# Performance work log

Measured on AMD Instinct MI355X. Metric: run time of the kernel, lower is better.

The kernel has to match this reference:

```python
import jax, jax.numpy as jnp
import numpy as np

NEG_BIG = -9e15

def setup_inputs() -> dict:
    key = jax.random.key(0)
    k1, k2, k3, k4 = jax.random.split(key, 4)
    N, F_in, F_out = 8192, 512, 128
    return {
        "input": jax.random.normal(k1, (N, F_in), dtype=jnp.float32),
        "adj": jax.random.randint(k2, (N, N), 0, 2, dtype=jnp.int32),
        "W": jax.random.normal(k3, (F_in, F_out), dtype=jnp.float32) * 0.05,
        "a": jax.random.normal(k4, (2 * F_out, 1), dtype=jnp.float32) * 0.05,
    }

def reference(input, adj, W, a):
    alpha = 0.2  # LeakyReLU negative slope
    h = input @ W                      # [N, F_out]
    F_out = h.shape[1]
    # concat score decomposition: a^T [h_i || h_j] = h_i @ a1 + h_j @ a2
    a1 = a[:F_out, 0]                  # [F_out]
    a2 = a[F_out:, 0]                  # [F_out]
    e = jax.nn.leaky_relu(h @ a1[:, None] + (h @ a2)[None, :], negative_slope=alpha)  # [N, N]
    e = jnp.where(adj > 0, e, NEG_BIG)
    attention = jax.nn.softmax(e, axis=1)
    h_prime = attention @ h            # [N, F_out]
    return jax.nn.elu(h_prime)         # concat=True
```

## Files before the change

### kernel.cpp

```cpp
#include <hip/hip_runtime.h>
#include <hip/hip_bf16.h>


typedef __attribute__((ext_vector_type(4))) float f32x4;
typedef __attribute__((ext_vector_type(8))) short s16x8;

#define N_NODES 8192
#define F_IN 512
#define F_OUT 128
#define JS 16
#define WCOLS (N_NODES / JS)

static __device__ __forceinline__ short f2bf(float f) {
  __hip_bfloat16 h = __float2bfloat16(f);
  return __builtin_bit_cast(short, h);
}

__global__ __launch_bounds__(256) void k_mask(const int* __restrict__ adj,
    unsigned long long* __restrict__ mask) {
  const int nwaves = gridDim.x * 4;
  int wid = blockIdx.x * 4 + (threadIdx.x >> 6);
  int lane = threadIdx.x & 63;
  const int ntasks = N_NODES * (N_NODES / 256);
  for (int task = wid; task < ntasks; task += nwaves) {
    int row = task >> 5;
    int cg = task & 31;
    const int* p = adj + (size_t)row * N_NODES + cg * 256 + lane;
    int v0 = p[0], v1 = p[64], v2 = p[128], v3 = p[192];
    unsigned long long b0 = __ballot(v0 != 0);
    unsigned long long b1 = __ballot(v1 != 0);
    unsigned long long b2 = __ballot(v2 != 0);
    unsigned long long b3 = __ballot(v3 != 0);
    if (lane == 0) {
      unsigned long long* q = mask + (size_t)row * (N_NODES / 64) + cg * 4;
      ulonglong2 w0; w0.x = b0; w0.y = b1;
      ulonglong2 w1; w1.x = b2; w1.y = b3;
      *(ulonglong2*)(q) = w0;
      *(ulonglong2*)(q + 2) = w1;
    }
  }
}

__global__ void k0a_wt(const float* __restrict__ W, unsigned short* __restrict__ WT) {
  int idx = blockIdx.x * 256 + threadIdx.x;
  int k = idx >> 7, f = idx & 127;
  WT[(size_t)f * F_IN + k] = (unsigned short)f2bf(W[idx]);
}

__global__ void k0c_wa(const float* __restrict__ W, const float* __restrict__ a,
                       float* __restrict__ wa) {
  int k = blockIdx.x * 256 + threadIdx.x;
  if (k >= F_IN) return;
  const float* Wr = W + (size_t)k * F_OUT;
  float d1 = 0.f, d2 = 0.f;
#pragma unroll 8
  for (int f = 0; f < F_OUT; f += 4) {
    f32x4 w  = *(const f32x4*)(Wr + f);
    f32x4 a1 = *(const f32x4*)(a + f);
    f32x4 a2 = *(const f32x4*)(a + F_OUT + f);
    d1 += w[0] * a1[0] + w[1] * a1[1] + w[2] * a1[2] + w[3] * a1[3];
    d2 += w[0] * a2[0] + w[1] * a2[1] + w[2] * a2[2] + w[3] * a2[3];
  }
  wa[k] = d1;
  wa[F_IN + k] = d2;
}

__global__ __launch_bounds__(256) void k0b_x(const float* __restrict__ X,
    const float* __restrict__ wa, unsigned short* __restrict__ Xb,
    f32x4* __restrict__ rowdat, unsigned* __restrict__ pE) {
  int wave = threadIdx.x >> 6, lane = threadIdx.x & 63;
  int i = blockIdx.x * 4 + wave;
  const float* Xr = X + (size_t)i * F_IN + lane * 8;
  f32x4 x0 = ((const f32x4*)Xr)[0];
  f32x4 x1 = ((const f32x4*)Xr)[1];
  f32x4 w10 = ((const f32x4*)(wa + lane * 8))[0];
  f32x4 w11 = ((const f32x4*)(wa + lane * 8))[1];
  f32x4 w20 = ((const f32x4*)(wa + F_IN + lane * 8))[0];
  f32x4 w21 = ((const f32x4*)(wa + F_IN + lane * 8))[1];

  s16x8 xb;
#pragma unroll
  for (int e = 0; e < 4; e++) { xb[e] = f2bf(x0[e]); xb[e + 4] = f2bf(x1[e]); }
  *(s16x8*)(Xb + (size_t)i * F_IN + lane * 8) = xb;

  float d1 = 0.f, d2 = 0.f;
#pragma unroll
  for (int e = 0; e < 4; e++) {
    d1 += x0[e] * w10[e] + x1[e] * w11[e];
    d2 += x0[e] * w20[e] + x1[e] * w21[e];
  }
#pragma unroll
  for (int m = 1; m < 64; m <<= 1) {
    d1 += __shfl_xor(d1, m, 64);
    d2 += __shfl_xor(d2, m, 64);
  }
  if (lane == 0) {
    float s1 = d1, s2 = d2;
    f32x4 rd;
    rd[0] = expf(s1);
    rd[1] = expf(0.2f * s1);
    rd[2] = expf(-s1);
    rd[3] = 0.f;
    rowdat[i] = rd;
    unsigned e2  = (unsigned)(unsigned short)f2bf(expf(s2));
    unsigned e2s = (unsigned)(unsigned short)f2bf(expf(0.2f * s2));
    pE[i] = (e2s << 16) | e2;
  }
}

__global__ __launch_bounds__(256) void k1_gemm(const unsigned short* __restrict__ WT,
    const unsigned short* __restrict__ Xb, unsigned short* __restrict__ hT) {
  int wave = threadIdx.x >> 6, lane = threadIdx.x & 63;
  int lrow = lane & 15, grp = lane >> 4;
  int tile = blockIdx.x * 4 + wave;
  int fb = tile & 7;
  int nb = tile >> 3;

  const unsigned short* Ar = WT + (size_t)(fb * 16 + lrow) * F_IN + grp * 8;
  const unsigned short* Br = Xb + (size_t)(nb * 16 + lrow) * F_IN + grp * 8;

  f32x4 acc = (f32x4)(0.0f);
#pragma unroll
  for (int k0 = 0; k0 < F_IN; k0 += 32) {
    s16x8 af = *(const s16x8*)(Ar + k0);
    s16x8 bf = *(const s16x8*)(Br + k0);
    acc = __builtin_amdgcn_mfma_f32_16x16x32_bf16(af, bf, acc, 0, 0, 0);
  }
#pragma unroll
  for (int r = 0; r < 4; r++)
    hT[(size_t)(fb * 16 + grp * 4 + r) * N_NODES + nb * 16 + lrow] =
        (unsigned short)f2bf(acc[r]);
}

__global__ __launch_bounds__(256, 2) void k2_main(const unsigned* __restrict__ mask32,
    const unsigned short* __restrict__ hT, const f32x4* __restrict__ rowdat,
    const unsigned* __restrict__ pE, float* __restrict__ accws,
    float* __restrict__ denws) {
  int wave = threadIdx.x >> 6, lane = threadIdx.x & 63;
  int lrow = lane & 15, grp = lane >> 4;
  int rb = blockIdx.x >> 2;
  int js = (blockIdx.x & 3) * 4 + wave;
  int rbase = rb * 64;
  int jlo = js * WCOLS;

  float E1[4], E1s[4], T1[4];
#pragma unroll
  for (int rt = 0; rt < 4; rt++) {
    f32x4 rd = rowdat[rbase + rt * 16 + lrow];
    E1[rt] = rd[0]; E1s[rt] = rd[1]; T1[rt] = rd[2];
  }

  f32x4 acc[4][8];
#pragma unroll
  for (int rt = 0; rt < 4; rt++)
#pragma unroll
    for (int n = 0; n < 8; n++) acc[rt][n] = (f32x4)(0.0f);
  float dsum[4] = {0.f, 0.f, 0.f, 0.f};

#define PROC1(rt, pe, e)                                              \
  {                                                                   \
    unsigned pu = (pe);                                               \
    float E2  = __builtin_bit_cast(float, pu << 16);                  \
    float E2s = __builtin_bit_cast(float, pu & 0xffff0000u);          \
    float sel = (E2 > T1[rt]) ? E1[rt] * E2 : E1s[rt] * E2s;          \
    float p = ((b >> (e)) & 1u) ? sel : 0.f;                          \
    dsum[rt] += p;                                                    \
    af[rt][e] = f2bf(p);                                              \
  }

  for (int sc = 0; sc < 4; sc++) {
    int jb = jlo + sc * 128;
    uint4 mm[4];
#pragma unroll
    for (int rt = 0; rt < 4; rt++)
      mm[rt] = *(const uint4*)(mask32 +
          (size_t)(rbase + rt * 16 + lrow) * (N_NODES / 32) + jb / 32);

#pragma unroll
    for (int t = 0; t < 4; t++) {
      int jj = jb + t * 32 + grp * 8;
      const uint4* pp = (const uint4*)(pE + jj);
      uint4 P0 = pp[0], P1 = pp[1];
      s16x8 af[4];
#pragma unroll
      for (int rt = 0; rt < 4; rt++) {
        unsigned b = (mm[rt][t] >> (grp * 8)) & 0xffu;
        PROC1(rt, P0.x, 0); PROC1(rt, P0.y, 1);
        PROC1(rt, P0.z, 2); PROC1(rt, P0.w, 3);
        PROC1(rt, P1.x, 4); PROC1(rt, P1.y, 5);
        PROC1(rt, P1.z, 6); PROC1(rt, P1.w, 7);
      }
#pragma unroll
      for (int n = 0; n < 8; n++) {
        s16x8 bf = *(const s16x8*)(hT + (size_t)(n * 16 + lrow) * N_NODES + jj);
#pragma unroll
        for (int rt = 0; rt < 4; rt++)
          acc[rt][n] =
              __builtin_amdgcn_mfma_f32_16x16x32_bf16(af[rt], bf, acc[rt][n], 0, 0, 0);
      }
    }
  }
#undef PROC1

#pragma unroll
  for (int rt = 0; rt < 4; rt++) {
    float d = dsum[rt];
    d += __shfl_xor(d, 16, 64);
    d += __shfl_xor(d, 32, 64);
    if (lane < 16) denws[js * N_NODES + rbase + rt * 16 + lane] = d;
  }

#pragma unroll
  for (int rt = 0; rt < 4; rt++)
#pragma unroll
    for (int n = 0; n < 8; n++)
#pragma unroll
      for (int r = 0; r < 4; r++)
        accws[((size_t)js * N_NODES + rbase + rt * 16 + grp * 4 + r) * F_OUT +
              n * 16 + lrow] = acc[rt][n][r];
}

__global__ void k3_fin(const float* __restrict__ accws,
                       const float* __restrict__ denws, float* __restrict__ out) {
  int idx4 = blockIdx.x * 256 + threadIdx.x;
  int i = idx4 >> 5;
  const int S4 = N_NODES * F_OUT / 4;
  f32x4 s = (f32x4)(0.0f);
  float d = 0.f;
#pragma unroll
  for (int js = 0; js < JS; js++) {
    s += ((const f32x4*)accws)[idx4 + (size_t)js * S4];
    d += denws[i + js * N_NODES];
  }
  f32x4 v = s / d;
#pragma unroll
  for (int e = 0; e < 4; e++) v[e] = v[e] > 0.f ? v[e] : expm1f(v[e]);
  ((f32x4*)out)[idx4] = v;
}

extern "C" void kernel_launch(void* const* d_in, const int* in_sizes, int n_in,
                              void* d_out, int out_size, void* d_ws, size_t ws_size,
                              hipStream_t stream) {
  const float* X   = (const float*)d_in[0];
  const int*   adj = (const int*)d_in[1];
  const float* W   = (const float*)d_in[2];
  const float* a   = (const float*)d_in[3];
  float* out = (float*)d_out;

  char* ws = (char*)d_ws;
  size_t off = 0;
  unsigned short* WT = (unsigned short*)(ws + off); off += (size_t)F_OUT * F_IN * 2;
  unsigned short* Xb = (unsigned short*)(ws + off); off += (size_t)N_NODES * F_IN * 2;
  unsigned short* hT = (unsigned short*)(ws + off); off += (size_t)F_OUT * N_NODES * 2;
  f32x4* rowdat = (f32x4*)(ws + off); off += (size_t)N_NODES * 16;
  unsigned* pE = (unsigned*)(ws + off); off += (size_t)N_NODES * 4;
  float* wa = (float*)(ws + off); off += (size_t)2 * F_IN * 4;
  unsigned long long* mask = (unsigned long long*)(ws + off);
  off += (size_t)N_NODES * (N_NODES / 64) * 8;
  float* accws = (float*)(ws + off); off += (size_t)JS * N_NODES * F_OUT * 4;
  float* denws = (float*)(ws + off); off += (size_t)JS * N_NODES * 4;
  (void)in_sizes; (void)n_in; (void)out_size; (void)ws_size;

  k_mask<<<2048, 256, 0, stream>>>(adj, mask);
  k0a_wt<<<(F_IN * F_OUT) / 256, 256, 0, stream>>>(W, WT);
  k0c_wa<<<2, 256, 0, stream>>>(W, a, wa);
  k0b_x<<<N_NODES / 4, 256, 0, stream>>>(X, wa, Xb, rowdat, pE);
  k1_gemm<<<1024, 256, 0, stream>>>(WT, Xb, hT);
  k2_main<<<(N_NODES / 64) * (JS / 4), 256, 0, stream>>>((const unsigned*)mask, hT,
                                                         rowdat, pE, accws, denws);
  k3_fin<<<(N_NODES * F_OUT) / 4 / 256, 256, 0, stream>>>(accws, denws, out);
}
```

Measured before the change: 535.8 us.

## Merge prep kernels, drop Xb staging, reduce split-K partials in shared memory

The seven launches become four. The W transpose and the W·a product share one kernel, and the adjacency mask, the row scores and the h GEMM run as disjoint block ranges of a second kernel. The GEMM now reads fp32 X and converts it to bf16 in registers, which removes the Xb buffer and its round trip through memory. The main kernel sums its four waves' partial accumulators in LDS before writing, cutting the accws/denws traffic and the final reduction from 16 slices to 4, at the cost of added LDS and __syncthreads in the epilogue. Merging the mask pass with the GEMM lets them overlap, but the GEMM blocks now redo the fp32 loads and conversions for each feature tile.

```diff
diff --git a/kernel.cpp b/kernel.cpp
--- a/kernel.cpp
+++ b/kernel.cpp
@@ -16,130 +16,132 @@
   return __builtin_bit_cast(short, h);
 }
 
-__global__ __launch_bounds__(256) void k_mask(const int* __restrict__ adj,
-    unsigned long long* __restrict__ mask) {
-  const int nwaves = gridDim.x * 4;
-  int wid = blockIdx.x * 4 + (threadIdx.x >> 6);
-  int lane = threadIdx.x & 63;
-  const int ntasks = N_NODES * (N_NODES / 256);
-  for (int task = wid; task < ntasks; task += nwaves) {
-    int row = task >> 5;
-    int cg = task & 31;
-    const int* p = adj + (size_t)row * N_NODES + cg * 256 + lane;
-    int v0 = p[0], v1 = p[64], v2 = p[128], v3 = p[192];
-    unsigned long long b0 = __ballot(v0 != 0);
-    unsigned long long b1 = __ballot(v1 != 0);
-    unsigned long long b2 = __ballot(v2 != 0);
-    unsigned long long b3 = __ballot(v3 != 0);
+__global__ __launch_bounds__(256) void kA(const float* __restrict__ W,
+    const float* __restrict__ a, unsigned short* __restrict__ WT,
+    float* __restrict__ wa) {
+  int b = blockIdx.x;
+  if (b < 256) {
+    int idx = b * 256 + threadIdx.x;
+    int k = idx >> 7, f = idx & 127;
+    WT[(size_t)f * F_IN + k] = (unsigned short)f2bf(W[idx]);
+  } else {
+    int k = (b - 256) * 256 + threadIdx.x;
+    if (k < F_IN) {
+      const float* Wr = W + (size_t)k * F_OUT;
+      float d1 = 0.f, d2 = 0.f;
+#pragma unroll 8
+      for (int f = 0; f < F_OUT; f += 4) {
+        f32x4 w  = *(const f32x4*)(Wr + f);
+        f32x4 a1 = *(const f32x4*)(a + f);
+        f32x4 a2 = *(const f32x4*)(a + F_OUT + f);
+        d1 += w[0] * a1[0] + w[1] * a1[1] + w[2] * a1[2] + w[3] * a1[3];
+        d2 += w[0] * a2[0] + w[1] * a2[1] + w[2] * a2[2] + w[3] * a2[3];
+      }
+      wa[k] = d1;
+      wa[F_IN + k] = d2;
+    }
+  }
+}
+
+__global__ __launch_bounds__(256) void kB(const int* __restrict__ adj,
+    unsigned long long* __restrict__ mask, const float* __restrict__ X,
+    const float* __restrict__ wa, const unsigned short* __restrict__ WT,
+    f32x4* __restrict__ rowdat, unsigned* __restrict__ pE,
+    unsigned short* __restrict__ hT) {
+  int b = blockIdx.x;
+  int wave = threadIdx.x >> 6, lane = threadIdx.x & 63;
+
+  if (b < 4096) {
+    const int nwaves = 4096 * 4;
+    int wid = b * 4 + wave;
+    const int ntasks = N_NODES * (N_NODES / 256);
+    for (int task = wid; task < ntasks; task += nwaves) {
+      int row = task >> 5;
+      int cg = task & 31;
+      const int* p = adj + (size_t)row * N_NODES + cg * 256 + lane;
+      int v0 = p[0], v1 = p[64], v2 = p[128], v3 = p[192];
+      unsigned long long b0 = __ballot(v0 != 0);
+      unsigned long long b1 = __ballot(v1 != 0);
+      unsigned long long b2 = __ballot(v2 != 0);
+      unsigned long long b3 = __ballot(v3 != 0);
+      if (lane == 0) {
+        unsigned long long* q = mask + (size_t)row * (N_NODES / 64) + cg * 4;
+        ulonglong2 w0; w0.x = b0; w0.y = b1;
+        ulonglong2 w1; w1.x = b2; w1.y = b3;
+        *(ulonglong2*)(q) = w0;
+        *(ulonglong2*)(q + 2) = w1;
+      }
+    }
+  } else if (b < 6144) {
+    int i = (b - 4096) * 4 + wave;
+    const float* Xr = X + (size_t)i * F_IN + lane * 8;
+    f32x4 x0 = ((const f32x4*)Xr)[0];
+    f32x4 x1 = ((const f32x4*)Xr)[1];
+    f32x4 w10 = ((const f32x4*)(wa + lane * 8))[0];
+    f32x4 w11 = ((const f32x4*)(wa + lane * 8))[1];
+    f32x4 w20 = ((const f32x4*)(wa + F_IN + lane * 8))[0];
+    f32x4 w21 = ((const f32x4*)(wa + F_IN + lane * 8))[1];
+    float d1 = 0.f, d2 = 0.f;
+#pragma unroll
+    for (int e = 0; e < 4; e++) {
+      d1 += x0[e] * w10[e] + x1[e] * w11[e];
+      d2 += x0[e] * w20[e] + x1[e] * w21[e];
+    }
+#pragma unroll
+    for (int m = 1; m < 64; m <<= 1) {
+      d1 += __shfl_xor(d1, m, 64);
+      d2 += __shfl_xor(d2, m, 64);
+    }
     if (lane == 0) {
-      unsigned long long* q = mask + (size_t)row * (N_NODES / 64) + cg * 4;
-      ulonglong2 w0; w0.x = b0; w0.y = b1;
-      ulonglong2 w1; w1.x = b2; w1.y = b3;
-      *(ulonglong2*)(q) = w0;
-      *(ulonglong2*)(q + 2) = w1;
-    }
-  }
-}
-
-__global__ void k0a_wt(const float* __restrict__ W, unsigned short* __restrict__ WT) {
-  int idx = blockIdx.x * 256 + threadIdx.x;
-  int k = idx >> 7, f = idx & 127;
-  WT[(size_t)f * F_IN + k] = (unsigned short)f2bf(W[idx]);
-}
-
-__global__ void k0c_wa(const float* __restrict__ W, const float* __restrict__ a,
-                       float* __restrict__ wa) {
-  int k = blockIdx.x * 256 + threadIdx.x;
-  if (k >= F_IN) return;
-  const float* Wr = W + (size_t)k * F_OUT;
-  float d1 = 0.f, d2 = 0.f;
-#pragma unroll 8
-  for (int f = 0; f < F_OUT; f += 4) {
-    f32x4 w  = *(const f32x4*)(Wr + f);
-    f32x4 a1 = *(const f32x4*)(a + f);
-    f32x4 a2 = *(const f32x4*)(a + F_OUT + f);
-    d1 += w[0] * a1[0] + w[1] * a1[1] + w[2] * a1[2] + w[3] * a1[3];
-    d2 += w[0] * a2[0] + w[1] * a2[1] + w[2] * a2[2] + w[3] * a2[3];
-  }
-  wa[k] = d1;
-  wa[F_IN + k] = d2;
-}
-
-__global__ __launch_bounds__(256) void k0b_x(const float* __restrict__ X,
-    const float* __restrict__ wa, unsigned short* __restrict__ Xb,
-    f32x4* __restrict__ rowdat, unsigned* __restrict__ pE) {
-  int wave = threadIdx.x >> 6, lane = threadIdx.x & 63;
-  int i = blockIdx.x * 4 + wave;
-  const float* Xr = X + (size_t)i * F_IN + lane * 8;
-  f32x4 x0 = ((const f32x4*)Xr)[0];
-  f32x4 x1 = ((const f32x4*)Xr)[1];
-  f32x4 w10 = ((const f32x4*)(wa + lane * 8))[0];
-  f32x4 w11 = ((const f32x4*)(wa + lane * 8))[1];
-  f32x4 w20 = ((const f32x4*)(wa + F_IN + lane * 8))[0];
-  f32x4 w21 = ((const f32x4*)(wa + F_IN + lane * 8))[1];
-
-  s16x8 xb;
-#pragma unroll
-  for (int e = 0; e < 4; e++) { xb[e] = f2bf(x0[e]); xb[e + 4] = f2bf(x1[e]); }
-  *(s16x8*)(Xb + (size_t)i * F_IN + lane * 8) = xb;
-
-  float d1 = 0.f, d2 = 0.f;
-#pragma unroll
-  for (int e = 0; e < 4; e++) {
-    d1 += x0[e] * w10[e] + x1[e] * w11[e];
-    d2 += x0[e] * w20[e] + x1[e] * w21[e];
-  }
-#pragma unroll
-  for (int m = 1; m < 64; m <<= 1) {
-    d1 += __shfl_xor(d1, m, 64);
-    d2 += __shfl_xor(d2, m, 64);
-  }
-  if (lane == 0) {
-    float s1 = d1, s2 = d2;
-    f32x4 rd;
-    rd[0] = expf(s1);
-    rd[1] = expf(0.2f * s1);
-    rd[2] = expf(-s1);
-    rd[3] = 0.f;
-    rowdat[i] = rd;
-    unsigned e2  = (unsigned)(unsigned short)f2bf(expf(s2));
-    unsigned e2s = (unsigned)(unsigned short)f2bf(expf(0.2f * s2));
-    pE[i] = (e2s << 16) | e2;
-  }
-}
-
-__global__ __launch_bounds__(256) void k1_gemm(const unsigned short* __restrict__ WT,
-    const unsigned short* __restrict__ Xb, unsigned short* __restrict__ hT) {
-  int wave = threadIdx.x >> 6, lane = threadIdx.x & 63;
-  int lrow = lane & 15, grp = lane >> 4;
-  int tile = blockIdx.x * 4 + wave;
-  int fb = tile & 7;
-  int nb = tile >> 3;
-
-  const unsigned short* Ar = WT + (size_t)(fb * 16 + lrow) * F_IN + grp * 8;
-  const unsigned short* Br = Xb + (size_t)(nb * 16 + lrow) * F_IN + grp * 8;
-
-  f32x4 acc = (f32x4)(0.0f);
-#pragma unroll
-  for (int k0 = 0; k0 < F_IN; k0 += 32) {
-    s16x8 af = *(const s16x8*)(Ar + k0);
-    s16x8 bf = *(const s16x8*)(Br + k0);
-    acc = __builtin_amdgcn_mfma_f32_16x16x32_bf16(af, bf, acc, 0, 0, 0);
-  }
-#pragma unroll
-  for (int r = 0; r < 4; r++)
-    hT[(size_t)(fb * 16 + grp * 4 + r) * N_NODES + nb * 16 + lrow] =
-        (unsigned short)f2bf(acc[r]);
-}
-
-__global__ __launch_bounds__(256, 2) void k2_main(const unsigned* __restrict__ mask32,
+      float s1 = d1, s2 = d2;
+      f32x4 rd;
+      rd[0] = expf(s1);
+      rd[1] = expf(0.2f * s1);
+      rd[2] = expf(-s1);
+      rd[3] = 0.f;
+      rowdat[i] = rd;
+      unsigned e2  = (unsigned)(unsigned short)f2bf(expf(s2));
+      unsigned e2s = (unsigned)(unsigned short)f2bf(expf(0.2f * s2));
+      pE[i] = (e2s << 16) | e2;
+    }
+  } else {
+    int lrow = lane & 15, grp = lane >> 4;
+    int tile = (b - 6144) * 4 + wave;
+    int fb = tile & 7;
+    int nb = tile >> 3;
+    const unsigned short* Ar = WT + (size_t)(fb * 16 + lrow) * F_IN + grp * 8;
+    const float* Br = X + (size_t)(nb * 16 + lrow) * F_IN + grp * 8;
+
+    f32x4 acc = (f32x4)(0.0f);
+#pragma unroll
+    for (int k0 = 0; k0 < F_IN; k0 += 32) {
+      s16x8 af = *(const s16x8*)(Ar + k0);
+      f32x4 b0 = *(const f32x4*)(Br + k0);
+      f32x4 b1 = *(const f32x4*)(Br + k0 + 4);
+      s16x8 bf;
+#pragma unroll
+      for (int e = 0; e < 4; e++) { bf[e] = f2bf(b0[e]); bf[e + 4] = f2bf(b1[e]); }
+      acc = __builtin_amdgcn_mfma_f32_16x16x32_bf16(af, bf, acc, 0, 0, 0);
+    }
+#pragma unroll
+    for (int r = 0; r < 4; r++)
+      hT[(size_t)(fb * 16 + grp * 4 + r) * N_NODES + nb * 16 + lrow] =
+          (unsigned short)f2bf(acc[r]);
+  }
+}
+
+__global__ __launch_bounds__(256, 2) void kC(const unsigned* __restrict__ mask32,
     const unsigned short* __restrict__ hT, const f32x4* __restrict__ rowdat,
     const unsigned* __restrict__ pE, float* __restrict__ accws,
     float* __restrict__ denws) {
+  __shared__ float red[4][16 * 132];
+  __shared__ float sden[4][4][16];
+
   int wave = threadIdx.x >> 6, lane = threadIdx.x & 63;
   int lrow = lane & 15, grp = lane >> 4;
   int rb = blockIdx.x >> 2;
-  int js = (blockIdx.x & 3) * 4 + wave;
+  int q = blockIdx.x & 3;
+  int js = q * 4 + wave;
   int rbase = rb * 64;
   int jlo = js * WCOLS;
 
@@ -163,7 +165,7 @@
     float E2  = __builtin_bit_cast(float, pu << 16);                  \
     float E2s = __builtin_bit_cast(float, pu & 0xffff0000u);          \
     float sel = (E2 > T1[rt]) ? E1[rt] * E2 : E1s[rt] * E2s;          \
-    float p = ((b >> (e)) & 1u) ? sel : 0.f;                          \
+    float p = ((bm >> (e)) & 1u) ? sel : 0.f;                         \
     dsum[rt] += p;                                                    \
     af[rt][e] = f2bf(p);                                              \
   }
@@ -184,7 +186,7 @@
       s16x8 af[4];
 #pragma unroll
       for (int rt = 0; rt < 4; rt++) {
-        unsigned b = (mm[rt][t] >> (grp * 8)) & 0xffu;
+        unsigned bm = (mm[rt][t] >> (grp * 8)) & 0xffu;
         PROC1(rt, P0.x, 0); PROC1(rt, P0.y, 1);
         PROC1(rt, P0.z, 2); PROC1(rt, P0.w, 3);
         PROC1(rt, P1.x, 4); PROC1(rt, P1.y, 5);
@@ -207,30 +209,50 @@
     float d = dsum[rt];
     d += __shfl_xor(d, 16, 64);
     d += __shfl_xor(d, 32, 64);
-    if (lane < 16) denws[js * N_NODES + rbase + rt * 16 + lane] = d;
-  }
-
-#pragma unroll
-  for (int rt = 0; rt < 4; rt++)
+    if (lane < 16) sden[wave][rt][lane] = d;
+  }
+
+#pragma unroll
+  for (int rt = 0; rt < 4; rt++) {
+    __syncthreads();
 #pragma unroll
     for (int n = 0; n < 8; n++)
 #pragma unroll
       for (int r = 0; r < 4; r++)
-        accws[((size_t)js * N_NODES + rbase + rt * 16 + grp * 4 + r) * F_OUT +
-              n * 16 + lrow] = acc[rt][n][r];
-}
-
-__global__ void k3_fin(const float* __restrict__ accws,
-                       const float* __restrict__ denws, float* __restrict__ out) {
+        red[wave][(grp * 4 + r) * 132 + n * 16 + lrow] = acc[rt][n][r];
+    __syncthreads();
+    int e0 = threadIdx.x * 8;
+    int row16 = e0 >> 7, col = e0 & 127;
+    int li = row16 * 132 + col;
+    f32x4 s0 = *(f32x4*)&red[0][li] + *(f32x4*)&red[1][li] +
+               *(f32x4*)&red[2][li] + *(f32x4*)&red[3][li];
+    f32x4 s1 = *(f32x4*)&red[0][li + 4] + *(f32x4*)&red[1][li + 4] +
+               *(f32x4*)&red[2][li + 4] + *(f32x4*)&red[3][li + 4];
+    float* dst = accws +
+        ((size_t)q * N_NODES + rbase + rt * 16 + row16) * F_OUT + col;
+    *(f32x4*)dst = s0;
+    *(f32x4*)(dst + 4) = s1;
+  }
+  __syncthreads();
+  if (threadIdx.x < 64) {
+    int rt = threadIdx.x >> 4, r16 = threadIdx.x & 15;
+    float d = sden[0][rt][r16] + sden[1][rt][r16] +
+              sden[2][rt][r16] + sden[3][rt][r16];
+    denws[q * N_NODES + rbase + threadIdx.x] = d;
+  }
+}
+
+__global__ void kD(const float* __restrict__ accws,
+                   const float* __restrict__ denws, float* __restrict__ out) {
   int idx4 = blockIdx.x * 256 + threadIdx.x;
   int i = idx4 >> 5;
   const int S4 = N_NODES * F_OUT / 4;
   f32x4 s = (f32x4)(0.0f);
   float d = 0.f;
 #pragma unroll
-  for (int js = 0; js < JS; js++) {
-    s += ((const f32x4*)accws)[idx4 + (size_t)js * S4];
-    d += denws[i + js * N_NODES];
+  for (int q = 0; q < 4; q++) {
+    s += ((const f32x4*)accws)[idx4 + (size_t)q * S4];
+    d += denws[i + q * N_NODES];
   }
   f32x4 v = s / d;
 #pragma unroll
@@ -250,23 +272,19 @@
   char* ws = (char*)d_ws;
   size_t off = 0;
   unsigned short* WT = (unsigned short*)(ws + off); off += (size_t)F_OUT * F_IN * 2;
-  unsigned short* Xb = (unsigned short*)(ws + off); off += (size_t)N_NODES * F_IN * 2;
   unsigned short* hT = (unsigned short*)(ws + off); off += (size_t)F_OUT * N_NODES * 2;
   f32x4* rowdat = (f32x4*)(ws + off); off += (size_t)N_NODES * 16;
   unsigned* pE = (unsigned*)(ws + off); off += (size_t)N_NODES * 4;
   float* wa = (float*)(ws + off); off += (size_t)2 * F_IN * 4;
   unsigned long long* mask = (unsigned long long*)(ws + off);
   off += (size_t)N_NODES * (N_NODES / 64) * 8;
-  float* accws = (float*)(ws + off); off += (size_t)JS * N_NODES * F_OUT * 4;
-  float* denws = (float*)(ws + off); off += (size_t)JS * N_NODES * 4;
+  float* accws = (float*)(ws + off); off += (size_t)4 * N_NODES * F_OUT * 4;
+  float* denws = (float*)(ws + off); off += (size_t)4 * N_NODES * 4;
   (void)in_sizes; (void)n_in; (void)out_size; (void)ws_size;
 
-  k_mask<<<2048, 256, 0, stream>>>(adj, mask);
-  k0a_wt<<<(F_IN * F_OUT) / 256, 256, 0, stream>>>(W, WT);
-  k0c_wa<<<2, 256, 0, stream>>>(W, a, wa);
-  k0b_x<<<N_NODES / 4, 256, 0, stream>>>(X, wa, Xb, rowdat, pE);
-  k1_gemm<<<1024, 256, 0, stream>>>(WT, Xb, hT);
-  k2_main<<<(N_NODES / 64) * (JS / 4), 256, 0, stream>>>((const unsigned*)mask, hT,
-                                                         rowdat, pE, accws, denws);
-  k3_fin<<<(N_NODES * F_OUT) / 4 / 256, 256, 0, stream>>>(accws, denws, out);
-}
+  kA<<<258, 256, 0, stream>>>(W, a, WT, wa);
+  kB<<<7168, 256, 0, stream>>>(adj, mask, X, wa, WT, rowdat, pE, hT);
+  kC<<<(N_NODES / 64) * 4, 256, 0, stream>>>((const unsigned*)mask, hT,
+                                             rowdat, pE, accws, denws);
+  kD<<<(N_NODES * F_OUT) / 4 / 256, 256, 0, stream>>>(accws, denws, out);
+}
```

After: 518.7 us. 3.2% less time.
